# Optimization experiments

Hardware: AMD Instinct MI355X
Metric: run time of the kernel (lower is better)

## Reference

```python
import jax, jax.numpy as jnp
import numpy as np

B, T = 64, 32768
N_PROT = 18          # protein channels (len(steady_state))
N_PROLIF = 12        # prolif-hill library terms
N_LIN = 18           # lin-hill library terms (== len(sigmoid_sign))
N_TERMS = 1 + N_PROLIF + N_LIN  # 31


def setup_inputs() -> dict:
    key = jax.random.key(0)
    ks = jax.random.split(key, 8)
    candidates = jax.random.uniform(ks[0], (B, T, 4 + N_PROT), dtype=jnp.float32)
    a = jax.random.normal(ks[1], (N_TERMS,), dtype=jnp.float32)
    steady_state = jax.random.uniform(ks[2], (N_PROT,), dtype=jnp.float32) * 0.5
    # +/-1 signs, mimicking the hard-coded sign vector in the original module
    sigmoid_sign = jnp.where(
        jax.random.bernoulli(ks[3], 0.5, (N_LIN,)), 1.0, -1.0
    ).astype(jnp.float32)
    K1 = jnp.array([0.5], dtype=jnp.float32)
    theta = jnp.array([2.0], dtype=jnp.float32)
    K2 = jnp.array([0.3], dtype=jnp.float32)
    # library indices: cols 0,1 of prolif and col 0 of lin index x (4 channels);
    # col 2 of prolif and col 1 of lin index proteins (18 channels)
    prolif_hill_idx = jnp.stack(
        [
            jax.random.randint(ks[4], (N_PROLIF,), 0, 4),
            jax.random.randint(jax.random.fold_in(ks[4], 1), (N_PROLIF,), 0, 4),
            jax.random.randint(jax.random.fold_in(ks[4], 2), (N_PROLIF,), 0, N_PROT),
        ],
        axis=1,
    ).astype(jnp.int32)
    lin_hill_idx = jnp.stack(
        [
            jax.random.randint(ks[5], (N_LIN,), 0, 4),
            jax.random.randint(jax.random.fold_in(ks[5], 1), (N_LIN,), 0, N_PROT),
        ],
        axis=1,
    ).astype(jnp.int32)
    self_propagate = jax.random.bernoulli(ks[6], 0.5, (N_TERMS,))
    return {
        "candidates": candidates,
        "a": a,
        "steady_state": steady_state,
        "sigmoid_sign": sigmoid_sign,
        "K1": K1,
        "theta": theta,
        "K2": K2,
        "prolif_hill_idx": prolif_hill_idx,
        "lin_hill_idx": lin_hill_idx,
        "self_propagate": self_propagate,
    }


def reference(candidates, a, steady_state, sigmoid_sign, K1, theta, K2,
              prolif_hill_idx, lin_hill_idx, self_propagate):
    con = candidates[:, :, 0:1]                       # [B,T,1]
    x3 = candidates[:, :, 1:4]                        # [B,T,3]
    proteins = candidates[:, :, 4:]                   # [B,T,18]
    d_prot = proteins - steady_state                  # [B,T,18]
    # augment x with its sum -> 4 channels
    x = jnp.concatenate([x3, jnp.sum(x3, axis=2, keepdims=True)], axis=2)

    # prolif-hill terms: Log_term(x_i, x_j) * Hill(K1, protein_k)
    p0 = x[:, :, prolif_hill_idx[:, 0]]
    p1 = x[:, :, prolif_hill_idx[:, 1]]
    p2 = proteins[:, :, prolif_hill_idx[:, 2]]
    prolif_hill = p0 * (1.0 - p1 / theta) * (p2 / (K1 + p2))  # [B,T,12]

    # lin-hill terms: x_i * Hill(K2, |d_prot_j|) * sharp_sigmoid(sign * d_prot_j)
    l0 = x[:, :, lin_hill_idx[:, 0]]
    dp = d_prot[:, :, lin_hill_idx[:, 1]]
    adp = jnp.abs(dp)
    sig = jax.nn.sigmoid(500.0 * (sigmoid_sign * dp - 0.05))
    lin_hill = l0 * (adp / (K2 + adp)) * sig                  # [B,T,18]

    terms = jnp.concatenate([con, prolif_hill, lin_hill], axis=2)  # [B,T,31]

    # masked zero-out: keep term i iff (self_propagate[i] and a[i] >= 0)
    # or (not self_propagate[i] and a[i] <= 0)
    keep = jnp.where(self_propagate, a >= 0.0, a <= 0.0)
    terms = terms * keep.astype(terms.dtype)

    return terms @ a  # [B,T]
```

## Files before the change

kernel.cpp:

```cpp
#include <hip/hip_runtime.h>

#define B_ 64
#define T_ 32768
#define NPROT 18
#define NPROLIF 12
#define NLIN 18
#define ROW 22
#define BLK 256
#define F4_PER_BLK (BLK*ROW/4)

#define AS1 __attribute__((address_space(1)))
#define AS3 __attribute__((address_space(3)))

__device__ __forceinline__ float sel4(unsigned i, float x0, float x1, float x2, float x3) {
    float lo = (i & 1u) ? x1 : x0;
    float hi = (i & 1u) ? x3 : x2;
    return (i & 2u) ? hi : lo;
}

__global__ __launch_bounds__(BLK) void sindy_kernel(
    const float* __restrict__ cand,
    const float* __restrict__ a,
    const float* __restrict__ ss,
    const float* __restrict__ sgn,
    const float* __restrict__ K1p,
    const float* __restrict__ thetap,
    const float* __restrict__ K2p,
    const int* __restrict__ pidx,
    const int* __restrict__ lidx,
    const int* __restrict__ sprop,
    float* __restrict__ out)
{
    __shared__ float sRow[BLK*ROW];
    __shared__ uint2 sPP[NPROLIF];
    __shared__ uint4 sLP[NLIN];
    __shared__ float sScal[4];

    const int tid = threadIdx.x;
    const int wbase = tid & ~63;

    const float4* g4 = reinterpret_cast<const float4*>(cand)
                       + (long long)blockIdx.x * F4_PER_BLK;
    float4* s4 = reinterpret_cast<float4*>(sRow);
    #pragma unroll
    for (int k = 0; k < 5; ++k) {
        __builtin_amdgcn_global_load_lds(
            (const AS1 void*)(g4 + k*BLK + tid),
            (AS3 void*)(s4 + k*BLK + wbase), 16, 0, 0);
    }
    if (tid < F4_PER_BLK - 5*BLK) {
        __builtin_amdgcn_global_load_lds(
            (const AS1 void*)(g4 + 5*BLK + tid),
            (AS3 void*)(s4 + 5*BLK + wbase), 16, 0, 0);
    }

    if (tid < NPROLIF) {
        int i = tid;
        int ia = pidx[i*3+0], ib = pidx[i*3+1], ic = pidx[i*3+2];
        float av = a[1+i];
        bool keep = sprop[1+i] ? (av >= 0.f) : (av <= 0.f);
        unsigned offs = (unsigned)ia | ((unsigned)ib << 2) | ((unsigned)(16 + ic*4) << 8);
        sPP[i] = make_uint2(offs, __float_as_uint(keep ? av : 0.f));
    } else if (tid < NPROLIF + NLIN) {
        int j = tid - NPROLIF;
        int i0 = lidx[j*2+0], i1 = lidx[j*2+1];
        float av = a[1+NPROLIF+j];
        bool keep = sprop[1+NPROLIF+j] ? (av >= 0.f) : (av <= 0.f);
        unsigned offs = (unsigned)i0 | ((unsigned)(16 + i1*4) << 8);
        sLP[j] = make_uint4(offs,
                            __float_as_uint(keep ? av : 0.f),
                            __float_as_uint(500.f * sgn[j]),
                            __float_as_uint(ss[i1]));
    } else if (tid == NPROLIF + NLIN) {
        float av = a[0];
        bool keep = sprop[0] ? (av >= 0.f) : (av <= 0.f);
        sScal[0] = K1p[0];
        sScal[1] = 1.0f / thetap[0];
        sScal[2] = K2p[0];
        sScal[3] = keep ? av : 0.f;
    }

    __syncthreads();

    const char* row = (const char*)&sRow[tid*ROW];
    float con = sRow[tid*ROW+0];
    float x0  = sRow[tid*ROW+1];
    float x1  = sRow[tid*ROW+2];
    float x2  = sRow[tid*ROW+3];
    float xs  = x0 + x1 + x2;

    const float K1 = sScal[0], invTh = sScal[1], K2 = sScal[2];
    float acc = sScal[3] * con;

    #pragma unroll
    for (int i = 0; i < NPROLIF; ++i) {
        uint2 pp = sPP[i];
        float coef = __uint_as_float(pp.y);
        float pA = sel4(pp.x & 3u, x0, x1, x2, xs);
        float pB = sel4((pp.x >> 2) & 3u, x0, x1, x2, xs);
        float pC = *(const float*)(row + ((pp.x >> 8) & 0xffu));
        float h  = pC * __builtin_amdgcn_rcpf(K1 + pC);
        acc += coef * (pA * (1.0f - pB * invTh) * h);
    }

    #pragma unroll
    for (int j = 0; j < NLIN; ++j) {
        uint4 lp = sLP[j];
        float coef = __uint_as_float(lp.y);
        float A    = __uint_as_float(lp.z);
        float ssv  = __uint_as_float(lp.w);
        float l0 = sel4(lp.x & 3u, x0, x1, x2, xs);
        float pr = *(const float*)(row + ((lp.x >> 8) & 0xffu));
        float dp  = pr - ssv;
        float adp = fabsf(dp);
        float h   = adp * __builtin_amdgcn_rcpf(K2 + adp);
        float z   = A * dp - 25.0f;
        float e   = __expf(-z);
        float sig = __builtin_amdgcn_rcpf(1.0f + e);
        acc += coef * (l0 * h * sig);
    }

    out[(long long)blockIdx.x * BLK + tid] = acc;
}

extern "C" void kernel_launch(void* const* d_in, const int* in_sizes, int n_in,
                              void* d_out, int out_size, void* d_ws, size_t ws_size,
                              hipStream_t stream) {
    const float* cand = (const float*)d_in[0];
    const float* a    = (const float*)d_in[1];
    const float* ss   = (const float*)d_in[2];
    const float* sgn  = (const float*)d_in[3];
    const float* K1   = (const float*)d_in[4];
    const float* th   = (const float*)d_in[5];
    const float* K2   = (const float*)d_in[6];
    const int*   pidx = (const int*)d_in[7];
    const int*   lidx = (const int*)d_in[8];
    const int*   sp   = (const int*)d_in[9];
    float* out = (float*)d_out;

    const int nblocks = (B_ * T_) / BLK;
    hipLaunchKernelGGL(sindy_kernel, dim3(nblocks), dim3(BLK), 0, stream,
                       cand, a, ss, sgn, K1, th, K2, pidx, lidx, sp, out);
}
```

Baseline: 44.62 us.

## Convert to persistent grid with double-buffered async global-to-LDS slab loads

Replaces the one-block-per-slab launch with a persistent grid of 768 blocks, each looping over slabs. The next slab's global-to-LDS load is issued into a second buffer while the current one is computed, with waitcnt and barriers controlling reuse. The goal is to hide memory latency and cut per-block setup (parameter tables) and launch tail. Risks are lower occupancy from twice the LDS and the barrier overhead added on each iteration.

Measured after the change: 51.50 us. 15.4% more time.

```diff
diff --git a/kernel.cpp b/kernel.cpp
--- a/kernel.cpp
+++ b/kernel.cpp
@@ -1,13 +1,12 @@
 #include <hip/hip_runtime.h>
 
-#define B_ 64
-#define T_ 32768
-#define NPROT 18
 #define NPROLIF 12
 #define NLIN 18
 #define ROW 22
 #define BLK 256
-#define F4_PER_BLK (BLK*ROW/4)
+#define F4_PER_SLAB (BLK*ROW/4)
+#define NSLAB 8192
+#define GRID 768
 
 #define AS1 __attribute__((address_space(1)))
 #define AS3 __attribute__((address_space(3)))
@@ -31,28 +30,16 @@
     const int* __restrict__ sprop,
     float* __restrict__ out)
 {
-    __shared__ float sRow[BLK*ROW];
+    __shared__ float sRow[2][BLK*ROW];
     __shared__ uint2 sPP[NPROLIF];
     __shared__ uint4 sLP[NLIN];
     __shared__ float sScal[4];
 
-    const int tid = threadIdx.x;
-    const int wbase = tid & ~63;
+    const int tid  = threadIdx.x;
+    const int bid  = blockIdx.x;
+    const int wave = tid >> 6;
 
-    const float4* g4 = reinterpret_cast<const float4*>(cand)
-                       + (long long)blockIdx.x * F4_PER_BLK;
-    float4* s4 = reinterpret_cast<float4*>(sRow);
-    #pragma unroll
-    for (int k = 0; k < 5; ++k) {
-        __builtin_amdgcn_global_load_lds(
-            (const AS1 void*)(g4 + k*BLK + tid),
-            (AS3 void*)(s4 + k*BLK + wbase), 16, 0, 0);
-    }
-    if (tid < F4_PER_BLK - 5*BLK) {
-        __builtin_amdgcn_global_load_lds(
-            (const AS1 void*)(g4 + 5*BLK + tid),
-            (AS3 void*)(s4 + 5*BLK + wbase), 16, 0, 0);
-    }
+    const int niter = (NSLAB - bid + GRID - 1) / GRID;
 
     if (tid < NPROLIF) {
         int i = tid;
@@ -80,47 +67,86 @@
         sScal[3] = keep ? av : 0.f;
     }
 
-    __syncthreads();
+    auto ISSUE = [&](int slab, int buf) {
+        const float4* g4 = reinterpret_cast<const float4*>(cand)
+                           + (long long)slab * F4_PER_SLAB;
+        float4* s4 = reinterpret_cast<float4*>(&sRow[buf][0]);
+        #pragma unroll
+        for (int k = 0; k < 5; ++k) {
+            __builtin_amdgcn_global_load_lds(
+                (const AS1 void*)(g4 + k*BLK + tid),
+                (AS3 void*)(s4 + k*BLK + (wave << 6)), 16, 0, 0);
+        }
+        const float* gf = (const float*)(g4 + 5*BLK);
+        float* sf = (float*)(s4 + 5*BLK);
+        __builtin_amdgcn_global_load_lds(
+            (const AS1 void*)(gf + tid),
+            (AS3 void*)(sf + (wave << 6)), 4, 0, 0);
+        __builtin_amdgcn_global_load_lds(
+            (const AS1 void*)(gf + 256 + tid),
+            (AS3 void*)(sf + 256 + (wave << 6)), 4, 0, 0);
+    };
 
-    const char* row = (const char*)&sRow[tid*ROW];
-    float con = sRow[tid*ROW+0];
-    float x0  = sRow[tid*ROW+1];
-    float x1  = sRow[tid*ROW+2];
-    float x2  = sRow[tid*ROW+3];
-    float xs  = x0 + x1 + x2;
+    ISSUE(bid, 0);
+    ISSUE(bid + GRID, 1);
 
-    const float K1 = sScal[0], invTh = sScal[1], K2 = sScal[2];
-    float acc = sScal[3] * con;
+    asm volatile("s_waitcnt lgkmcnt(0)" ::: "memory");
+    __builtin_amdgcn_s_barrier();
 
-    #pragma unroll
-    for (int i = 0; i < NPROLIF; ++i) {
-        uint2 pp = sPP[i];
-        float coef = __uint_as_float(pp.y);
-        float pA = sel4(pp.x & 3u, x0, x1, x2, xs);
-        float pB = sel4((pp.x >> 2) & 3u, x0, x1, x2, xs);
-        float pC = *(const float*)(row + ((pp.x >> 8) & 0xffu));
-        float h  = pC * __builtin_amdgcn_rcpf(K1 + pC);
-        acc += coef * (pA * (1.0f - pB * invTh) * h);
+    const float K1 = sScal[0], invTh = sScal[1], K2 = sScal[2], coef0 = sScal[3];
+
+    int buf = 0;
+    for (int i = 0; i < niter; ++i) {
+        if (i + 1 < niter) { asm volatile("s_waitcnt vmcnt(7)" ::: "memory"); }
+        else               { asm volatile("s_waitcnt vmcnt(0)" ::: "memory"); }
+        __builtin_amdgcn_sched_barrier(0);
+        __builtin_amdgcn_s_barrier();
+
+        const char* row = (const char*)&sRow[buf][tid*ROW];
+        float con = sRow[buf][tid*ROW+0];
+        float x0  = sRow[buf][tid*ROW+1];
+        float x1  = sRow[buf][tid*ROW+2];
+        float x2  = sRow[buf][tid*ROW+3];
+        float xs  = x0 + x1 + x2;
+
+        float acc = coef0 * con;
+
+        #pragma unroll
+        for (int t = 0; t < NPROLIF; ++t) {
+            uint2 pp = sPP[t];
+            float coef = __uint_as_float(pp.y);
+            float pA = sel4(pp.x & 3u, x0, x1, x2, xs);
+            float pB = sel4((pp.x >> 2) & 3u, x0, x1, x2, xs);
+            float pC = *(const float*)(row + ((pp.x >> 8) & 0xffu));
+            float h  = pC * __builtin_amdgcn_rcpf(K1 + pC);
+            acc += coef * (pA * (1.0f - pB * invTh) * h);
+        }
+
+        #pragma unroll
+        for (int t = 0; t < NLIN; ++t) {
+            uint4 lp = sLP[t];
+            float coef = __uint_as_float(lp.y);
+            float A    = __uint_as_float(lp.z);
+            float ssv  = __uint_as_float(lp.w);
+            float l0 = sel4(lp.x & 3u, x0, x1, x2, xs);
+            float pr = *(const float*)(row + ((lp.x >> 8) & 0xffu));
+            float dp  = pr - ssv;
+            float adp = fabsf(dp);
+            float h   = adp * __builtin_amdgcn_rcpf(K2 + adp);
+            float z   = A * dp - 25.0f;
+            float e   = __expf(-z);
+            float sig = __builtin_amdgcn_rcpf(1.0f + e);
+            acc += coef * (l0 * h * sig);
+        }
+
+        const int slab = bid + i * GRID;
+        out[(long long)slab * BLK + tid] = acc;
+
+        __builtin_amdgcn_s_barrier();
+        if (i + 2 < niter) ISSUE(bid + (i + 2) * GRID, buf);
+        buf ^= 1;
     }
 
-    #pragma unroll
-    for (int j = 0; j < NLIN; ++j) {
-        uint4 lp = sLP[j];
-        float coef = __uint_as_float(lp.y);
-        float A    = __uint_as_float(lp.z);
-        float ssv  = __uint_as_float(lp.w);
-        float l0 = sel4(lp.x & 3u, x0, x1, x2, xs);
-        float pr = *(const float*)(row + ((lp.x >> 8) & 0xffu));
-        float dp  = pr - ssv;
-        float adp = fabsf(dp);
-        float h   = adp * __builtin_amdgcn_rcpf(K2 + adp);
-        float z   = A * dp - 25.0f;
-        float e   = __expf(-z);
-        float sig = __builtin_amdgcn_rcpf(1.0f + e);
-        acc += coef * (l0 * h * sig);
-    }
-
-    out[(long long)blockIdx.x * BLK + tid] = acc;
 }
 
 extern "C" void kernel_launch(void* const* d_in, const int* in_sizes, int n_in,
@@ -138,7 +164,6 @@
     const int*   sp   = (const int*)d_in[9];
     float* out = (float*)d_out;
 
-    const int nblocks = (B_ * T_) / BLK;
-    hipLaunchKernelGGL(sindy_kernel, dim3(nblocks), dim3(BLK), 0, stream,
+    hipLaunchKernelGGL(sindy_kernel, dim3(GRID), dim3(BLK), 0, stream,
                        cand, a, ss, sgn, K1, th, K2, pidx, lidx, sp, out);
 }
```
